# Kernel tuning notes

Measured on AMD Instinct MI355X. Metric: run time of the kernel, lower is better.

Reference implementation:

```python
import jax, jax.numpy as jnp
import numpy as np

N, C, O, H, S, SHARE = 30000, 128, 128, 8, 16, 8
D = O // H            # mid_planes = 16
OS = O // SHARE       # 16
OFFSETS = [15000, 30000]
EPS = 1e-5


def _knn(p, offsets, k):
    """Exact per-batch KNN (incl. self), chunked to bound memory."""
    n = p.shape[0]
    idx = np.empty((n, k), dtype=np.int64)
    start = 0
    for end in offsets:
        pb = p[start:end]
        sq = (pb * pb).sum(-1)
        for qs in range(0, pb.shape[0], 1024):
            q = pb[qs:qs + 1024]
            d = sq[qs:qs + q.shape[0], None] - 2.0 * (q @ pb.T) + sq[None, :]
            part = np.argpartition(d, k - 1, axis=1)[:, :k]
            idx[start + qs:start + qs + q.shape[0]] = part + start
        start = end
    return idx


def _ln(x, g, b):
    m = x.mean(-1, keepdims=True)
    v = ((x - m) ** 2).mean(-1, keepdims=True)
    return (x - m) / jnp.sqrt(v + EPS) * g + b


def setup_inputs() -> dict:
    rng = np.random.default_rng(0)
    p_np = (rng.standard_normal((N, 3)) * 5.0).astype(np.float32)
    idx = _knn(p_np, OFFSETS, S)

    key = jax.random.key(0)
    ks = jax.random.split(key, 12)

    def lin(k, i, o):
        return (jax.random.normal(k, (i, o), jnp.float32) / np.sqrt(i)).astype(jnp.float32)

    return {
        "p": jnp.asarray(p_np),
        "x": jax.random.normal(ks[0], (N, C), jnp.float32),
        "idx": jnp.asarray(idx),
        "Wq": lin(ks[1], C, O), "bq": jnp.zeros((O,), jnp.float32),
        "Wk": lin(ks[2], C, O), "bk": jnp.zeros((O,), jnp.float32),
        "Wv": lin(ks[3], C, O), "bv": jnp.zeros((O,), jnp.float32),
        "Wp1": lin(ks[4], 3, 3), "bp1": jnp.zeros((3,), jnp.float32),
        "gp": jnp.ones((3,), jnp.float32), "betap": jnp.zeros((3,), jnp.float32),
        "Wp2": lin(ks[5], 3, O), "bp2": jnp.zeros((O,), jnp.float32),
        "gw1": jnp.ones((D,), jnp.float32), "betaw1": jnp.zeros((D,), jnp.float32),
        "Ww1": lin(ks[6], D, OS), "bw1": jnp.zeros((OS,), jnp.float32),
        "gw2": jnp.ones((OS,), jnp.float32), "betaw2": jnp.zeros((OS,), jnp.float32),
        "Ww2": lin(ks[7], OS, OS), "bw2": jnp.zeros((OS,), jnp.float32),
    }


def reference(p, x, idx, Wq, bq, Wk, bk, Wv, bv, Wp1, bp1, gp, betap, Wp2, bp2,
              gw1, betaw1, Ww1, bw1, gw2, betaw2, Ww2, bw2):
    xq = (x @ Wq + bq).reshape(N, H, D)          # (N,H,D)
    xk = x @ Wk + bk                              # (N,O)
    xv = x @ Wv + bv
    kg = xk[idx].reshape(N, S, H, D)              # neighbor gather
    vg = xv[idx].reshape(N, S, H, D)
    pr = p[idx] - p[:, None, :]                   # relative coords (N,S,3)
    pe = jax.nn.relu(_ln(pr @ Wp1 + bp1, gp, betap)) @ Wp2 + bp2  # (N,S,O)
    pe = pe.reshape(N, S, H, D)
    r = kg + pe - xq[:, None]                     # (N,S,H,D)
    w = jax.nn.relu(_ln(r, gw1, betaw1)) @ Ww1 + bw1
    w = jax.nn.relu(_ln(w, gw2, betaw2)) @ Ww2 + bw2  # (N,S,H,OS)
    w = jax.nn.softmax(w.mean(-1), axis=1)        # softmax over the S neighbors
    out = ((vg + pe) * w[..., None]).sum(axis=1)  # weighted neighbor reduce
    return out.reshape(N, O)
```

## Files before the change

### kernel.cpp

```cpp
#include <hip/hip_runtime.h>
#include <math.h>

typedef unsigned int  uint;
typedef unsigned short ushort;

constexpr int NPTS = 30000;
constexpr int NPAD = 30080;
constexpr int CIN  = 128;
constexpr int OC   = 128;
constexpr int NH   = 8;
constexpr int NS   = 16;
constexpr int DH   = 16;
constexpr int OSH  = 16;
constexpr float EPSF = 1e-5f;

typedef __attribute__((ext_vector_type(8))) short  bf16x8;
typedef __attribute__((ext_vector_type(4))) float  f32x4;
typedef __attribute__((ext_vector_type(2))) __fp16 h2;

__device__ __forceinline__ ushort f2bf(float f) {
    uint u = __float_as_uint(f);
    u += 0x7fff + ((u >> 16) & 1);
    return (ushort)(u >> 16);
}
__device__ __forceinline__ ushort f2h(float f) {
    __fp16 h = (__fp16)f;
    return *(ushort*)&h;
}
__device__ __forceinline__ uint pk2(float a, float b) {
    h2 v = __builtin_amdgcn_cvt_pkrtz(a, b);
    return *(uint*)&v;
}
__device__ __forceinline__ h2 asH2(uint u) { return *(h2*)&u; }

#if defined(__has_builtin)
#if __has_builtin(__builtin_elementwise_max)
#define PKMAX(a, b) __builtin_elementwise_max(a, b)
#endif
#endif
#ifndef PKMAX
__device__ __forceinline__ h2 PKMAX(h2 a, h2 b) {
    h2 r; r[0] = a[0] > b[0] ? a[0] : b[0]; r[1] = a[1] > b[1] ? a[1] : b[1]; return r;
}
#endif

constexpr int PK_WW1   = 0;
constexpr int PK_WP2   = 128;
constexpr int PK_BP2   = 320;
constexpr int PK_GW1   = 384;
constexpr int PK_BW1P  = 392;
constexpr int PK_GW2   = 400;
constexpr int PK_BW2P  = 408;
constexpr int PK_RM    = 416;
constexpr int PKF_BW1  = 424;
constexpr int PKF_RMB  = 440;

constexpr int XB_BLOCKS = (NPAD * CIN / 4) / 256;

__global__ __launch_bounds__(256) void prep_kernel(
    const float* __restrict__ x,
    const float* __restrict__ Wq, const float* __restrict__ Wk, const float* __restrict__ Wv,
    const float* __restrict__ Wp2, const float* __restrict__ bp2,
    const float* __restrict__ gw1, const float* __restrict__ betaw1,
    const float* __restrict__ Ww1, const float* __restrict__ bw1,
    const float* __restrict__ gw2, const float* __restrict__ betaw2,
    const float* __restrict__ Ww2, const float* __restrict__ bw2,
    ushort* __restrict__ xb, ushort* __restrict__ WT, uint* __restrict__ PK)
{
    const int b = blockIdx.x;
    const int t = threadIdx.x;
    if (b < XB_BLOCKS) {
        int e   = (b * 256 + t) * 4;
        int row = e >> 7;
        uint2 o = make_uint2(0, 0);
        if (row < NPTS) {
            float4 f = *(const float4*)(x + e);
            o.x = (uint)f2bf(f.x) | ((uint)f2bf(f.y) << 16);
            o.y = (uint)f2bf(f.z) | ((uint)f2bf(f.w) << 16);
        }
        *(uint2*)(xb + e) = o;
    } else if (b < XB_BLOCKS + 3) {
        int mat = b - XB_BLOCKS;
        const float* W = (mat == 0) ? Wq : (mat == 1 ? Wk : Wv);
        ushort* T = WT + mat * OC * CIN;
        if (t < OC) {
            for (int k = 0; k < CIN; ++k)
                T[t * CIN + k] = f2bf(W[k * OC + t]);
        }
    } else {
        float* FPK = (float*)PK;
        if (t < 128) {
            int dp = t >> 4, o = t & 15;
            PK[PK_WW1 + t] = pk2(Ww1[(2 * dp) * OSH + o], Ww1[(2 * dp + 1) * OSH + o]);
        }
        if (t < 192) {
            int c = t >> 6, jj = t & 63;
            PK[PK_WP2 + t] = pk2(Wp2[c * OC + 2 * jj], Wp2[c * OC + 2 * jj + 1]);
        }
        if (t < 64)
            PK[PK_BP2 + t] = pk2(bp2[2 * t], bp2[2 * t + 1]);
        if (t < 8) {
            PK[PK_GW1 + t]  = pk2(gw1[2 * t],    gw1[2 * t + 1]);
            PK[PK_BW1P + t] = pk2(betaw1[2 * t], betaw1[2 * t + 1]);
            PK[PK_GW2 + t]  = pk2(gw2[2 * t],    gw2[2 * t + 1]);
            PK[PK_BW2P + t] = pk2(betaw2[2 * t], betaw2[2 * t + 1]);
            float r0 = 0.f, r1 = 0.f;
            #pragma unroll
            for (int o2 = 0; o2 < OSH; ++o2) {
                r0 += Ww2[(2 * t) * OSH + o2];
                r1 += Ww2[(2 * t + 1) * OSH + o2];
            }
            PK[PK_RM + t] = pk2(r0 * (1.f / OSH), r1 * (1.f / OSH));
        }
        if (t < 16)
            FPK[PKF_BW1 + t] = bw1[t];
        if (t == 16) {
            float acc = 0.f;
            #pragma unroll
            for (int o2 = 0; o2 < OSH; ++o2) acc += bw2[o2];
            FPK[PKF_RMB] = acc * (1.f / OSH);
        }
    }
}

__global__ __launch_bounds__(256) void qkv_mfma(
    const ushort* __restrict__ xb, const ushort* __restrict__ WT,
    const float* __restrict__ bq, const float* __restrict__ bk, const float* __restrict__ bv,
    ushort* __restrict__ yq, ushort* __restrict__ yk, ushort* __restrict__ yv)
{
    const int mat = blockIdx.y;
    const float* bias = (mat == 0) ? bq : (mat == 1 ? bk : bv);
    ushort* y         = (mat == 0) ? yq : (mat == 1 ? yk : yv);
    const ushort* T   = WT + mat * OC * CIN;

    const int n0   = blockIdx.x * 128;
    const int t    = threadIdx.x;
    const int wave = t >> 6;
    const int lane = t & 63;
    const int m16  = lane & 15;
    const int quad = lane >> 4;

    f32x4 acc[2][8];
    #pragma unroll
    for (int mt = 0; mt < 2; ++mt)
        #pragma unroll
        for (int nt = 0; nt < 8; ++nt)
            acc[mt][nt] = (f32x4){0.f, 0.f, 0.f, 0.f};

    const ushort* arow0 = xb + (size_t)(n0 + wave * 32 + m16) * CIN;
    const ushort* arow1 = arow0 + 16 * CIN;

    #pragma unroll
    for (int ks = 0; ks < 4; ++ks) {
        const int kb = ks * 32 + quad * 8;
        bf16x8 a0 = *(const bf16x8*)(arow0 + kb);
        bf16x8 a1 = *(const bf16x8*)(arow1 + kb);
        #pragma unroll
        for (int nt = 0; nt < 8; ++nt) {
            bf16x8 bfr = *(const bf16x8*)(T + (size_t)(nt * 16 + m16) * CIN + kb);
            acc[0][nt] = __builtin_amdgcn_mfma_f32_16x16x32_bf16(a0, bfr, acc[0][nt], 0, 0, 0);
            acc[1][nt] = __builtin_amdgcn_mfma_f32_16x16x32_bf16(a1, bfr, acc[1][nt], 0, 0, 0);
        }
    }

    #pragma unroll
    for (int mt = 0; mt < 2; ++mt) {
        #pragma unroll
        for (int nt = 0; nt < 8; ++nt) {
            const int col = nt * 16 + m16;
            const float bcol = bias[col];
            #pragma unroll
            for (int r = 0; r < 4; ++r) {
                int row = n0 + wave * 32 + mt * 16 + quad * 4 + r;
                if (row < NPTS)
                    y[(size_t)row * OC + col] = f2h(acc[mt][nt][r] + bcol);
            }
        }
    }
}

__global__ __launch_bounds__(128) void attn_kernel(
    const float* __restrict__ p, const int* __restrict__ idx,
    const ushort* __restrict__ xq, const ushort* __restrict__ xk, const ushort* __restrict__ xv,
    const float* __restrict__ Wp1, const float* __restrict__ bp1,
    const float* __restrict__ gp,  const float* __restrict__ betap,
    const uint* __restrict__ PK,
    float* __restrict__ out)
{
    const int n = blockIdx.x;
    const int t = threadIdx.x;
    const int s = t & 15;
    const int h = t >> 4;

    const float* FPK = (const float*)PK;

    __shared__ uint s_c[NS][68];

    const int j = idx[n * NS + s];

    float t0, t1, t2;
    {
        float pr0 = p[j * 3 + 0] - p[n * 3 + 0];
        float pr1 = p[j * 3 + 1] - p[n * 3 + 1];
        float pr2 = p[j * 3 + 2] - p[n * 3 + 2];
        float u[3];
        #pragma unroll
        for (int c = 0; c < 3; ++c)
            u[c] = bp1[c] + pr0 * Wp1[0 * 3 + c] + pr1 * Wp1[1 * 3 + c] + pr2 * Wp1[2 * 3 + c];
        float m   = (u[0] + u[1] + u[2]) * (1.f / 3.f);
        float d0 = u[0] - m, d1 = u[1] - m, d2 = u[2] - m;
        float var = (d0 * d0 + d1 * d1 + d2 * d2) * (1.f / 3.f);
        float inv = rsqrtf(var + EPSF);
        t0 = fmaxf((u[0] - m) * inv * gp[0] + betap[0], 0.f);
        t1 = fmaxf((u[1] - m) * inv * gp[1] + betap[1], 0.f);
        t2 = fmaxf((u[2] - m) * inv * gp[2] + betap[2], 0.f);
    }

    const int obase = h * DH;

    __attribute__((aligned(16))) h2 pe2[8];
    {
        h2 t02 = asH2(pk2(t0, t0));
        h2 t12 = asH2(pk2(t1, t1));
        h2 t22 = asH2(pk2(t2, t2));
        const uint* W0p = PK + PK_WP2 + 0 * 64 + h * 8;
        const uint* W1p = PK + PK_WP2 + 1 * 64 + h * 8;
        const uint* W2p = PK + PK_WP2 + 2 * 64 + h * 8;
        const uint* Bp  = PK + PK_BP2 + h * 8;
        #pragma unroll
        for (int i = 0; i < 8; ++i) {
            h2 acc = asH2(Bp[i]);
            acc = acc + t02 * asH2(W0p[i]);
            acc = acc + t12 * asH2(W1p[i]);
            acc = acc + t22 * asH2(W2p[i]);
            pe2[i] = acc;
        }
    }

    __attribute__((aligned(16))) h2 v2[8], r2[8];
    {
        __attribute__((aligned(16))) h2 k2[8], q2[8];
        const uint4* k4 = (const uint4*)(xk + (size_t)j * OC + obase);
        const uint4* v4 = (const uint4*)(xv + (size_t)j * OC + obase);
        const uint4* q4 = (const uint4*)(xq + (size_t)n * OC + obase);
        *(uint4*)&k2[0] = k4[0]; *(uint4*)&k2[4] = k4[1];
        *(uint4*)&v2[0] = v4[0]; *(uint4*)&v2[4] = v4[1];
        *(uint4*)&q2[0] = q4[0]; *(uint4*)&q2[4] = q4[1];
        #pragma unroll
        for (int i = 0; i < 8; ++i)
            r2[i] = (k2[i] + pe2[i]) - q2[i];
    }

    __attribute__((aligned(16))) h2 a2[8];
    {
        h2 sum2 = r2[0];
        #pragma unroll
        for (int i = 1; i < 8; ++i) sum2 = sum2 + r2[i];
        float m = ((float)sum2[0] + (float)sum2[1]) * (1.f / DH);
        h2 m2 = asH2(pk2(m, m));
        h2 vs2 = {(__fp16)0.f, (__fp16)0.f};
        #pragma unroll
        for (int i = 0; i < 8; ++i) {
            r2[i] = r2[i] - m2;
            vs2 = vs2 + r2[i] * r2[i];
        }
        float var = ((float)vs2[0] + (float)vs2[1]) * (1.f / DH);
        float inv = rsqrtf(var + EPSF);
        h2 inv2 = asH2(pk2(inv, inv));
        h2 z2 = {(__fp16)0.f, (__fp16)0.f};
        #pragma unroll
        for (int i = 0; i < 8; ++i) {
            h2 gi = asH2(PK[PK_GW1 + i]) * inv2;
            a2[i] = PKMAX(r2[i] * gi + asH2(PK[PK_BW1P + i]), z2);
        }
    }

    float w1[OSH];
    #pragma unroll
    for (int o2 = 0; o2 < OSH; ++o2) w1[o2] = FPK[PKF_BW1 + o2];
    #pragma unroll
    for (int dp = 0; dp < 8; ++dp) {
        #pragma unroll
        for (int o2 = 0; o2 < OSH; ++o2)
            w1[o2] = __builtin_amdgcn_fdot2(a2[dp], asH2(PK[PK_WW1 + dp * 16 + o2]), w1[o2], false);
    }

    float logit;
    {
        __attribute__((aligned(16))) h2 w2[8];
        #pragma unroll
        for (int i = 0; i < 8; ++i) w2[i] = asH2(pk2(w1[2 * i], w1[2 * i + 1]));
        h2 sum2 = w2[0];
        #pragma unroll
        for (int i = 1; i < 8; ++i) sum2 = sum2 + w2[i];
        float m = ((float)sum2[0] + (float)sum2[1]) * (1.f / OSH);
        h2 m2 = asH2(pk2(m, m));
        h2 vs2 = {(__fp16)0.f, (__fp16)0.f};
        #pragma unroll
        for (int i = 0; i < 8; ++i) {
            w2[i] = w2[i] - m2;
            vs2 = vs2 + w2[i] * w2[i];
        }
        float var = ((float)vs2[0] + (float)vs2[1]) * (1.f / OSH);
        float inv = rsqrtf(var + EPSF);
        h2 inv2 = asH2(pk2(inv, inv));
        h2 z2 = {(__fp16)0.f, (__fp16)0.f};
        logit = FPK[PKF_RMB];
        #pragma unroll
        for (int i = 0; i < 8; ++i) {
            h2 gi = asH2(PK[PK_GW2 + i]) * inv2;
            h2 bv2 = PKMAX(w2[i] * gi + asH2(PK[PK_BW2P + i]), z2);
            logit = __builtin_amdgcn_fdot2(bv2, asH2(PK[PK_RM + i]), logit, false);
        }
    }

    float w;
    {
        float mx = logit;
        #pragma unroll
        for (int mask = 1; mask < 16; mask <<= 1)
            mx = fmaxf(mx, __shfl_xor(mx, mask));
        float e = __expf(logit - mx);
        float den = e;
        #pragma unroll
        for (int mask = 1; mask < 16; mask <<= 1)
            den += __shfl_xor(den, mask);
        w = e / den;
    }

    {
        h2 w2p = asH2(pk2(w, w));
        __attribute__((aligned(16))) h2 c2[8];
        #pragma unroll
        for (int i = 0; i < 8; ++i)
            c2[i] = (v2[i] + pe2[i]) * w2p;
        *(uint4*)&s_c[s][h * 8]     = *(uint4*)&c2[0];
        *(uint4*)&s_c[s][h * 8 + 4] = *(uint4*)&c2[4];
    }
    __syncthreads();

    {
        const int oh = t >> 4;
        const int od = t & 15;
        const int col = oh * 8 + (od >> 1);
        h2 acc2 = {(__fp16)0.f, (__fp16)0.f};
        #pragma unroll
        for (int ss = 0; ss < NS; ++ss)
            acc2 = acc2 + asH2(s_c[ss][col]);
        out[(size_t)n * OC + t] = (float)acc2[od & 1];
    }
}

extern "C" void kernel_launch(void* const* d_in, const int* in_sizes, int n_in,
                              void* d_out, int out_size, void* d_ws, size_t ws_size,
                              hipStream_t stream) {
    const float* p     = (const float*)d_in[0];
    const float* x     = (const float*)d_in[1];
    const int*   idx   = (const int*)d_in[2];
    const float* Wq    = (const float*)d_in[3];
    const float* bq    = (const float*)d_in[4];
    const float* Wk    = (const float*)d_in[5];
    const float* bk    = (const float*)d_in[6];
    const float* Wv    = (const float*)d_in[7];
    const float* bv    = (const float*)d_in[8];
    const float* Wp1   = (const float*)d_in[9];
    const float* bp1   = (const float*)d_in[10];
    const float* gp    = (const float*)d_in[11];
    const float* betap = (const float*)d_in[12];
    const float* Wp2   = (const float*)d_in[13];
    const float* bp2   = (const float*)d_in[14];
    const float* gw1   = (const float*)d_in[15];
    const float* betaw1= (const float*)d_in[16];
    const float* Ww1   = (const float*)d_in[17];
    const float* bw1   = (const float*)d_in[18];
    const float* gw2   = (const float*)d_in[19];
    const float* betaw2= (const float*)d_in[20];
    const float* Ww2   = (const float*)d_in[21];
    const float* bw2   = (const float*)d_in[22];
    float* out = (float*)d_out;

    ushort* xb = (ushort*)d_ws;
    ushort* WT = xb + (size_t)NPAD * CIN;
    ushort* xq = WT + 3 * OC * CIN;
    ushort* xk = xq + (size_t)NPTS * OC;
    ushort* xv = xk + (size_t)NPTS * OC;
    uint*   PACKS = (uint*)(xv + (size_t)NPTS * OC);

    prep_kernel<<<XB_BLOCKS + 4, 256, 0, stream>>>(x, Wq, Wk, Wv,
                                                   Wp2, bp2, gw1, betaw1,
                                                   Ww1, bw1, gw2, betaw2, Ww2, bw2,
                                                   xb, WT, PACKS);

    dim3 g1(NPAD / 128, 3);
    qkv_mfma<<<g1, 256, 0, stream>>>(xb, WT, bq, bk, bv, xq, xk, xv);

    attn_kernel<<<NPTS, 128, 0, stream>>>(p, idx, xq, xk, xv,
                                          Wp1, bp1, gp, betap,
                                          PACKS, out);
}
```

Baseline: 196.0 us.

## Fuse x conversion into QKV MFMA and switch GEMM to fp16

```diff
diff --git a/kernel.cpp b/kernel.cpp
--- a/kernel.cpp
+++ b/kernel.cpp
@@ -5,7 +5,6 @@
 typedef unsigned short ushort;
 
 constexpr int NPTS = 30000;
-constexpr int NPAD = 30080;
 constexpr int CIN  = 128;
 constexpr int OC   = 128;
 constexpr int NH   = 8;
@@ -14,15 +13,10 @@
 constexpr int OSH  = 16;
 constexpr float EPSF = 1e-5f;
 
-typedef __attribute__((ext_vector_type(8))) short  bf16x8;
+typedef __attribute__((ext_vector_type(8))) __fp16 h8;
 typedef __attribute__((ext_vector_type(4))) float  f32x4;
 typedef __attribute__((ext_vector_type(2))) __fp16 h2;
 
-__device__ __forceinline__ ushort f2bf(float f) {
-    uint u = __float_as_uint(f);
-    u += 0x7fff + ((u >> 16) & 1);
-    return (ushort)(u >> 16);
-}
 __device__ __forceinline__ ushort f2h(float f) {
     __fp16 h = (__fp16)f;
     return *(ushort*)&h;
@@ -55,38 +49,29 @@
 constexpr int PKF_BW1  = 424;
 constexpr int PKF_RMB  = 440;
 
-constexpr int XB_BLOCKS = (NPAD * CIN / 4) / 256;
-
 __global__ __launch_bounds__(256) void prep_kernel(
-    const float* __restrict__ x,
     const float* __restrict__ Wq, const float* __restrict__ Wk, const float* __restrict__ Wv,
     const float* __restrict__ Wp2, const float* __restrict__ bp2,
     const float* __restrict__ gw1, const float* __restrict__ betaw1,
     const float* __restrict__ Ww1, const float* __restrict__ bw1,
     const float* __restrict__ gw2, const float* __restrict__ betaw2,
     const float* __restrict__ Ww2, const float* __restrict__ bw2,
-    ushort* __restrict__ xb, ushort* __restrict__ WT, uint* __restrict__ PK)
+    ushort* __restrict__ WT, uint* __restrict__ PK)
 {
     const int b = blockIdx.x;
     const int t = threadIdx.x;
-    if (b < XB_BLOCKS) {
-        int e   = (b * 256 + t) * 4;
-        int row = e >> 7;
-        uint2 o = make_uint2(0, 0);
-        if (row < NPTS) {
-            float4 f = *(const float4*)(x + e);
-            o.x = (uint)f2bf(f.x) | ((uint)f2bf(f.y) << 16);
-            o.y = (uint)f2bf(f.z) | ((uint)f2bf(f.w) << 16);
-        }
-        *(uint2*)(xb + e) = o;
-    } else if (b < XB_BLOCKS + 3) {
-        int mat = b - XB_BLOCKS;
+    if (b < 24) {
+        const int mat = b >> 3;
+        const int cg  = b & 7;
         const float* W = (mat == 0) ? Wq : (mat == 1 ? Wk : Wv);
-        ushort* T = WT + mat * OC * CIN;
-        if (t < OC) {
-            for (int k = 0; k < CIN; ++k)
-                T[t * CIN + k] = f2bf(W[k * OC + t]);
-        }
+        const int col = cg * 16 + (t >> 4);
+        const int k0  = (t & 15) * 8;
+        float v0 = W[(k0 + 0) * OC + col], v1 = W[(k0 + 1) * OC + col];
+        float v2 = W[(k0 + 2) * OC + col], v3 = W[(k0 + 3) * OC + col];
+        float v4 = W[(k0 + 4) * OC + col], v5 = W[(k0 + 5) * OC + col];
+        float v6 = W[(k0 + 6) * OC + col], v7 = W[(k0 + 7) * OC + col];
+        uint4 u = make_uint4(pk2(v0, v1), pk2(v2, v3), pk2(v4, v5), pk2(v6, v7));
+        *(uint4*)&WT[(size_t)mat * OC * CIN + (size_t)col * CIN + k0] = u;
     } else {
         float* FPK = (float*)PK;
         if (t < 128) {
@@ -124,14 +109,14 @@
 }
 
 __global__ __launch_bounds__(256) void qkv_mfma(
-    const ushort* __restrict__ xb, const ushort* __restrict__ WT,
+    const float* __restrict__ x, const ushort* __restrict__ WT,
     const float* __restrict__ bq, const float* __restrict__ bk, const float* __restrict__ bv,
     ushort* __restrict__ yq, ushort* __restrict__ yk, ushort* __restrict__ yv)
 {
     const int mat = blockIdx.y;
     const float* bias = (mat == 0) ? bq : (mat == 1 ? bk : bv);
     ushort* y         = (mat == 0) ? yq : (mat == 1 ? yk : yv);
-    const ushort* T   = WT + mat * OC * CIN;
+    const ushort* T   = WT + (size_t)mat * OC * CIN;
 
     const int n0   = blockIdx.x * 128;
     const int t    = threadIdx.x;
@@ -147,19 +132,31 @@
         for (int nt = 0; nt < 8; ++nt)
             acc[mt][nt] = (f32x4){0.f, 0.f, 0.f, 0.f};
 
-    const ushort* arow0 = xb + (size_t)(n0 + wave * 32 + m16) * CIN;
-    const ushort* arow1 = arow0 + 16 * CIN;
+    int r0i = n0 + wave * 32 + m16;
+    int r1i = r0i + 16;
+    if (r0i > NPTS - 1) r0i = NPTS - 1;
+    if (r1i > NPTS - 1) r1i = NPTS - 1;
+    const float* arow0 = x + (size_t)r0i * CIN;
+    const float* arow1 = x + (size_t)r1i * CIN;
 
     #pragma unroll
     for (int ks = 0; ks < 4; ++ks) {
         const int kb = ks * 32 + quad * 8;
-        bf16x8 a0 = *(const bf16x8*)(arow0 + kb);
-        bf16x8 a1 = *(const bf16x8*)(arow1 + kb);
+        float4 f00 = *(const float4*)(arow0 + kb);
+        float4 f01 = *(const float4*)(arow0 + kb + 4);
+        float4 f10 = *(const float4*)(arow1 + kb);
+        float4 f11 = *(const float4*)(arow1 + kb + 4);
+        uint4 ua0 = make_uint4(pk2(f00.x, f00.y), pk2(f00.z, f00.w),
+                               pk2(f01.x, f01.y), pk2(f01.z, f01.w));
+        uint4 ua1 = make_uint4(pk2(f10.x, f10.y), pk2(f10.z, f10.w),
+                               pk2(f11.x, f11.y), pk2(f11.z, f11.w));
+        h8 a0 = *(h8*)&ua0;
+        h8 a1 = *(h8*)&ua1;
         #pragma unroll
         for (int nt = 0; nt < 8; ++nt) {
-            bf16x8 bfr = *(const bf16x8*)(T + (size_t)(nt * 16 + m16) * CIN + kb);
-            acc[0][nt] = __builtin_amdgcn_mfma_f32_16x16x32_bf16(a0, bfr, acc[0][nt], 0, 0, 0);
-            acc[1][nt] = __builtin_amdgcn_mfma_f32_16x16x32_bf16(a1, bfr, acc[1][nt], 0, 0, 0);
+            h8 bfr = *(const h8*)(T + (size_t)(nt * 16 + m16) * CIN + kb);
+            acc[0][nt] = __builtin_amdgcn_mfma_f32_16x16x32_f16(a0, bfr, acc[0][nt], 0, 0, 0);
+            acc[1][nt] = __builtin_amdgcn_mfma_f32_16x16x32_f16(a1, bfr, acc[1][nt], 0, 0, 0);
         }
     }
 
@@ -325,7 +322,7 @@
         #pragma unroll
         for (int mask = 1; mask < 16; mask <<= 1)
             den += __shfl_xor(den, mask);
-        w = e / den;
+        w = e * __builtin_amdgcn_rcpf(den);
     }
 
     {
@@ -379,20 +376,19 @@
     const float* bw2   = (const float*)d_in[22];
     float* out = (float*)d_out;
 
-    ushort* xb = (ushort*)d_ws;
-    ushort* WT = xb + (size_t)NPAD * CIN;
+    ushort* WT = (ushort*)d_ws;
     ushort* xq = WT + 3 * OC * CIN;
     ushort* xk = xq + (size_t)NPTS * OC;
     ushort* xv = xk + (size_t)NPTS * OC;
     uint*   PACKS = (uint*)(xv + (size_t)NPTS * OC);
 
-    prep_kernel<<<XB_BLOCKS + 4, 256, 0, stream>>>(x, Wq, Wk, Wv,
-                                                   Wp2, bp2, gw1, betaw1,
-                                                   Ww1, bw1, gw2, betaw2, Ww2, bw2,
-                                                   xb, WT, PACKS);
-
-    dim3 g1(NPAD / 128, 3);
-    qkv_mfma<<<g1, 256, 0, stream>>>(xb, WT, bq, bk, bv, xq, xk, xv);
+    prep_kernel<<<25, 256, 0, stream>>>(Wq, Wk, Wv,
+                                        Wp2, bp2, gw1, betaw1,
+                                        Ww1, bw1, gw2, betaw2, Ww2, bw2,
+                                        WT, PACKS);
+
+    dim3 g1((NPTS + 127) / 128, 3);
+    qkv_mfma<<<g1, 256, 0, stream>>>(x, WT, bq, bk, bv, xq, xk, xv);
 
     attn_kernel<<<NPTS, 128, 0, stream>>>(p, idx, xq, xk, xv,
                                           Wp1, bp1, gp, betap,
```

Measured after the change: 188.0 us, median of 2. 4.1% less time.
